# Kernel tuning notes

Measured on AMD Instinct MI355X. Metric: run time of the kernel, lower is better.

## Reference

```python
import jax, jax.numpy as jnp
import numpy as np


def setup_inputs() -> dict:
    key = jax.random.key(0)
    ks = jax.random.split(key, 12)
    B, T, E, H, D, NB, BS = 64, 1, 1280, 20, 64, 7, 64
    w = lambda k: jax.random.normal(k, (E, E), jnp.float32) * 0.02
    return {
        "hidden_states": jax.random.normal(ks[0], (B, T, E), jnp.float32),
        "kcache": jax.random.normal(ks[1], (B, H, NB, BS, D), jnp.float32),
        "vcache": jax.random.normal(ks[2], (B, H, NB, BS, D), jnp.float32),
        "wq": w(ks[3]), "bq": jax.random.normal(ks[4], (E,), jnp.float32) * 0.02,
        "wk": w(ks[5]), "bk": jnp.zeros((E,), jnp.float32),
        "wv": w(ks[6]), "bv": jax.random.normal(ks[7], (E,), jnp.float32) * 0.02,
        "wo": w(ks[8]), "bo": jax.random.normal(ks[9], (E,), jnp.float32) * 0.02,
        "cache_position": jax.random.randint(ks[10], (B,), 0, 447, jnp.int32),
        "block_tables": jax.random.randint(ks[11], (B, NB), 0, NB, jnp.int32),
    }


def reference(hidden_states, kcache, vcache, wq, bq, wk, bk, wv, bv, wo, bo,
              cache_position, block_tables):
    B, T, E = hidden_states.shape          # T == 1 (decode)
    _, H, NB, BS, D = kcache.shape
    L = NB * BS                             # max logical cache length (448)
    scaling = D ** -0.5

    # projections -> (B, H, T, D)
    q = (hidden_states @ wq.T + bq).reshape(B, T, H, D).transpose(0, 2, 1, 3) * scaling
    kn = (hidden_states @ wk.T + bk).reshape(B, T, H, D).transpose(0, 2, 1, 3)
    vn = (hidden_states @ wv.T + bv).reshape(B, T, H, D).transpose(0, 2, 1, 3)

    # paged block-table gather: logical cache (B, H, L, D)
    bt = block_tables[:, None, :, None, None].astype(jnp.int32)
    kc = jnp.take_along_axis(kcache, bt, axis=2).reshape(B, H, L, D)
    vc = jnp.take_along_axis(vcache, bt, axis=2).reshape(B, H, L, D)

    # insert the new token's k/v at position cache_position[b]
    pos = jnp.arange(L, dtype=jnp.int32)
    seq = cache_position.reshape(B, 1, 1, 1)
    at_new = pos.reshape(1, 1, L, 1) == seq          # (B,1,L,1)
    k_full = jnp.where(at_new, kn, kc)               # kn (B,H,1,D) broadcasts
    v_full = jnp.where(at_new, vn, vc)

    # causal decode: attend to positions <= cache_position
    scores = jnp.einsum('bhtd,bhld->bhtl', q, k_full)
    valid = pos.reshape(1, 1, 1, L) <= cache_position.reshape(B, 1, 1, 1)
    scores = jnp.where(valid, scores, jnp.finfo(scores.dtype).min)
    probs = jax.nn.softmax(scores, axis=-1)
    out = jnp.einsum('bhtl,bhld->bhtd', probs, v_full)

    out = out.transpose(0, 2, 1, 3).reshape(B, T, E)
    return out @ wo.T + bo
```

## Files before the change

### kernel.cpp

```cpp
#include <hip/hip_runtime.h>
#include <math.h>

#define E 1280
#define NHEAD 20
#define HD 64
#define NBLK 7
#define NB 64

typedef __bf16 bf16x8 __attribute__((ext_vector_type(8)));
typedef __bf16 bf16x4 __attribute__((ext_vector_type(4)));
typedef float floatx4 __attribute__((ext_vector_type(4)));

__device__ __forceinline__ float wave_max64(float v) {
    #pragma unroll
    for (int o = 32; o > 0; o >>= 1) v = fmaxf(v, __shfl_xor(v, o, 64));
    return v;
}
__device__ __forceinline__ float wave_sum64(float v) {
    #pragma unroll
    for (int o = 32; o > 0; o >>= 1) v += __shfl_xor(v, o, 64);
    return v;
}

template<int NTOT, bool QKV>
__global__ __launch_bounds__(256) void mfma_gemm(
    const float* __restrict__ A,
    const float* __restrict__ W0, const float* __restrict__ W1,
    const float* __restrict__ W2,
    const float* __restrict__ b0, const float* __restrict__ b1,
    const float* __restrict__ b2,
    float* __restrict__ C)
{
    __shared__ __align__(16) __bf16 Asl[64][72];
    __shared__ __align__(16) __bf16 Wsl[16][72];

    const int t = threadIdx.x;
    const int lane = t & 63;
    const int wv = t >> 6;
    const int quad = lane >> 4;
    const int l16 = lane & 15;
    const int jg0 = blockIdx.x * 16;

    int j0; const float* Wp; const float* bp; float scl;
    if (QKV) {
        const int msel = jg0 / E;
        j0 = jg0 - msel * E;
        Wp = (msel == 0) ? W0 : ((msel == 1) ? W1 : W2);
        bp = (msel == 0) ? b0 : ((msel == 1) ? b1 : b2);
        scl = (msel == 0) ? 0.125f : 1.0f;
    } else { j0 = jg0; Wp = W0; bp = b0; scl = 1.0f; }

    const int srow = t >> 4;
    const int sc4 = t & 15;

    floatx4 acc = {0.f, 0.f, 0.f, 0.f};

    for (int k0 = 0; k0 < E; k0 += 64) {
        float4 a4[4];
        #pragma unroll
        for (int r = 0; r < 4; ++r)
            a4[r] = *(const float4*)&A[(size_t)(r * 16 + srow) * E + k0 + sc4 * 4];
        float4 w4 = *(const float4*)&Wp[(size_t)(j0 + srow) * E + k0 + sc4 * 4];

        __syncthreads();
        #pragma unroll
        for (int r = 0; r < 4; ++r) {
            bf16x4 p;
            p[0] = (__bf16)a4[r].x; p[1] = (__bf16)a4[r].y;
            p[2] = (__bf16)a4[r].z; p[3] = (__bf16)a4[r].w;
            *(bf16x4*)&Asl[r * 16 + srow][sc4 * 4] = p;
        }
        {
            bf16x4 p;
            p[0] = (__bf16)w4.x; p[1] = (__bf16)w4.y;
            p[2] = (__bf16)w4.z; p[3] = (__bf16)w4.w;
            *(bf16x4*)&Wsl[srow][sc4 * 4] = p;
        }
        __syncthreads();

        bf16x8 af0 = *(const bf16x8*)&Asl[16 * wv + l16][quad * 8];
        bf16x8 bf0 = *(const bf16x8*)&Wsl[l16][quad * 8];
        acc = __builtin_amdgcn_mfma_f32_16x16x32_bf16(af0, bf0, acc, 0, 0, 0);
        bf16x8 af1 = *(const bf16x8*)&Asl[16 * wv + l16][32 + quad * 8];
        bf16x8 bf1 = *(const bf16x8*)&Wsl[l16][32 + quad * 8];
        acc = __builtin_amdgcn_mfma_f32_16x16x32_bf16(af1, bf1, acc, 0, 0, 0);
    }

    const float bj = bp[j0 + l16];
    #pragma unroll
    for (int r = 0; r < 4; ++r) {
        const int row = 16 * wv + quad * 4 + r;
        C[(size_t)row * NTOT + jg0 + l16] = (acc[r] + bj) * scl;
    }
}

__global__ __launch_bounds__(256) void attn_kernel(
    const float* __restrict__ qkv,
    const float* __restrict__ kcache, const float* __restrict__ vcache,
    const int* __restrict__ cache_position, const int* __restrict__ block_tables,
    float* __restrict__ obuf)
{
    const int bh = blockIdx.x;
    const int b = bh / NHEAD;
    const int h = bh % NHEAD;
    const int lane = threadIdx.x & 63;
    const int wv = threadIdx.x >> 6;
    const int d4 = lane & 15;
    const int sg = lane >> 4;

    __shared__ __align__(16) float q_lds[64];
    __shared__ __align__(16) float o_lds[4][64];
    __shared__ float ml_lds[4][2];

    const int pos = cache_position[b];
    const int last = pos - 1;
    const int col = h * HD + lane;

    const float qd  = qkv[(size_t)b * (3 * E) + col];
    const float knd = qkv[(size_t)b * (3 * E) + E + col];
    const float vnd = qkv[(size_t)b * (3 * E) + 2 * E + col];
    if (wv == 0) q_lds[lane] = qd;
    __syncthreads();

    float m = -INFINITY, lsum = 0.0f;
    float4 vacc = make_float4(0.f, 0.f, 0.f, 0.f);

    for (int nb = wv; nb * 64 <= last; nb += 4) {
        const int phys = block_tables[b * NBLK + nb];
        const size_t boff = ((size_t)((b * NHEAD + h) * NBLK + phys)) << 12;
        const float* __restrict__ Kb = kcache + boff;
        const float* __restrict__ Vb = vcache + boff;

        float sc = 0.0f;
        const float4* Krow = (const float4*)(Kb + lane * HD);
        #pragma unroll
        for (int dd = 0; dd < 16; ++dd) {
            float4 k4 = Krow[dd];
            float4 q4 = ((const float4*)q_lds)[dd];
            sc = fmaf(k4.x, q4.x, sc);
            sc = fmaf(k4.y, q4.y, sc);
            sc = fmaf(k4.z, q4.z, sc);
            sc = fmaf(k4.w, q4.w, sc);
        }
        const int l = nb * 64 + lane;
        if (l > last) sc = -INFINITY;

        const float bm = wave_max64(sc);
        const float mnew = fmaxf(m, bm);
        const float alpha = __expf(m - mnew);
        const float p = __expf(sc - mnew);
        lsum = lsum * alpha + wave_sum64(p);
        vacc.x *= alpha; vacc.y *= alpha; vacc.z *= alpha; vacc.w *= alpha;

        #pragma unroll
        for (int j = 0; j < 16; ++j) {
            const int s = sg + 4 * j;
            const float ps = __shfl(p, s, 64);
            float4 v4 = *(const float4*)&Vb[s * HD + d4 * 4];
            vacc.x = fmaf(ps, v4.x, vacc.x);
            vacc.y = fmaf(ps, v4.y, vacc.y);
            vacc.z = fmaf(ps, v4.z, vacc.z);
            vacc.w = fmaf(ps, v4.w, vacc.w);
        }
        m = mnew;
    }

    #pragma unroll
    for (int o = 16; o <= 32; o <<= 1) {
        vacc.x += __shfl_xor(vacc.x, o, 64);
        vacc.y += __shfl_xor(vacc.y, o, 64);
        vacc.z += __shfl_xor(vacc.z, o, 64);
        vacc.w += __shfl_xor(vacc.w, o, 64);
    }
    if (sg == 0) *(float4*)&o_lds[wv][d4 * 4] = vacc;
    if (lane == 0) { ml_lds[wv][0] = m; ml_lds[wv][1] = lsum; }
    __syncthreads();

    if (wv == 0) {
        const float qk = wave_sum64(qd * knd);
        float Mf = qk;
        #pragma unroll
        for (int w = 0; w < 4; ++w) Mf = fmaxf(Mf, ml_lds[w][0]);
        float osum = 0.0f, Ls = 0.0f;
        #pragma unroll
        for (int w = 0; w < 4; ++w) {
            const float f = __expf(ml_lds[w][0] - Mf);
            osum = fmaf(o_lds[w][lane], f, osum);
            Ls   = fmaf(ml_lds[w][1], f, Ls);
        }
        const float pn = __expf(qk - Mf);
        osum = fmaf(pn, vnd, osum);
        Ls += pn;
        obuf[(size_t)b * E + h * HD + lane] = osum / Ls;
    }
}

extern "C" void kernel_launch(void* const* d_in, const int* in_sizes, int n_in,
                              void* d_out, int out_size, void* d_ws, size_t ws_size,
                              hipStream_t stream) {
    const float* hidden = (const float*)d_in[0];
    const float* kcache = (const float*)d_in[1];
    const float* vcache = (const float*)d_in[2];
    const float* wq = (const float*)d_in[3];
    const float* bq = (const float*)d_in[4];
    const float* wk = (const float*)d_in[5];
    const float* bk = (const float*)d_in[6];
    const float* wvp = (const float*)d_in[7];
    const float* bv = (const float*)d_in[8];
    const float* wo = (const float*)d_in[9];
    const float* bo = (const float*)d_in[10];
    const int* cpos = (const int*)d_in[11];
    const int* btab = (const int*)d_in[12];
    float* out = (float*)d_out;

    float* ws = (float*)d_ws;
    float* qkv = ws;
    float* ob  = ws + 64 * 3 * E;

    mfma_gemm<3 * E, true><<<(3 * E) / 16, 256, 0, stream>>>(
        hidden, wq, wk, wvp, bq, bk, bv, qkv);
    attn_kernel<<<NB * NHEAD, 256, 0, stream>>>(qkv, kcache, vcache, cpos, btab, ob);
    mfma_gemm<E, false><<<E / 16, 256, 0, stream>>>(
        ob, wo, wo, wo, bo, bo, bo, out);
}
```

Measured before the change: 350.8 us.

## Split K across waves in MFMA GEMM with per-wave LDS and final reduction

Each of the four waves in the projection GEMM now handles its own quarter of the K dimension, covering all 64 rows of A with four accumulators. Each wave stages data in a private LDS slice, so the per-iteration block-wide barriers go away. The partial sums are combined through LDS once at the end, and bias and scale are applied there. The trade-off is smaller per-row global load segments (less coalescing), a larger LDS footprint, and an extra reduction step; an empty leftover loop is also left in the code.

```diff
diff --git a/kernel.cpp b/kernel.cpp
--- a/kernel.cpp
+++ b/kernel.cpp
@@ -20,6 +20,12 @@
     #pragma unroll
     for (int o = 32; o > 0; o >>= 1) v += __shfl_xor(v, o, 64);
     return v;
+}
+
+__device__ __forceinline__ bf16x4 cvt4(float4 v) {
+    bf16x4 p;
+    p[0] = (__bf16)v.x; p[1] = (__bf16)v.y; p[2] = (__bf16)v.z; p[3] = (__bf16)v.w;
+    return p;
 }
 
 template<int NTOT, bool QKV>
@@ -31,8 +37,8 @@
     const float* __restrict__ b2,
     float* __restrict__ C)
 {
-    __shared__ __align__(16) __bf16 Asl[64][72];
-    __shared__ __align__(16) __bf16 Wsl[16][72];
+    __shared__ __align__(16) __bf16 Asl[4][64][72];
+    __shared__ __align__(16) __bf16 Wsl[4][16][72];
 
     const int t = threadIdx.x;
     const int lane = t & 63;
@@ -50,47 +56,62 @@
         scl = (msel == 0) ? 0.125f : 1.0f;
     } else { j0 = jg0; Wp = W0; bp = b0; scl = 1.0f; }
 
-    const int srow = t >> 4;
-    const int sc4 = t & 15;
-
-    floatx4 acc = {0.f, 0.f, 0.f, 0.f};
-
-    for (int k0 = 0; k0 < E; k0 += 64) {
-        float4 a4[4];
+    const int sr = lane >> 2;
+    const int sc = lane & 3;
+
+    floatx4 acc[4] = {};
+
+    const int kbeg = wv * (E / 4);
+    for (int c = 0; c < 5; ++c) {
+        const int k0 = kbeg + c * 64;
+        #pragma unroll
+        for (int rg = 0; rg < 4; ++rg) {
+            #pragma unroll
+            for (int cg = 0; cg < 4; ++cg) {
+                float4 v = *(const float4*)&A[(size_t)(rg * 16 + sr) * E + k0 + cg * 16 + sc * 4];
+                *(bf16x4*)&Asl[wv][rg * 16 + sr][cg * 16 + sc * 4] = cvt4(v);
+            }
+        }
+        #pragma unroll
+        for (int cg = 0; cg < 4; ++cg) {
+            float4 v = *(const float4*)&Wp[(size_t)(j0 + sr) * E + k0 + cg * 16 + sc * 4];
+            *(bf16x4*)&Wsl[wv][sr][cg * 16 + sc * 4] = cvt4(v);
+        }
+        bf16x8 bfr0 = *(const bf16x8*)&Wsl[wv][l16][quad * 8];
+        bf16x8 bfr1 = *(const bf16x8*)&Wsl[wv][l16][32 + quad * 8];
+        #pragma unroll
+        for (int rg = 0; rg < 4; ++rg) {
+            bf16x8 af0 = *(const bf16x8*)&Asl[wv][rg * 16 + l16][quad * 8];
+            acc[rg] = __builtin_amdgcn_mfma_f32_16x16x32_bf16(af0, bfr0, acc[rg], 0, 0, 0);
+            bf16x8 af1 = *(const bf16x8*)&Asl[wv][rg * 16 + l16][32 + quad * 8];
+            acc[rg] = __builtin_amdgcn_mfma_f32_16x16x32_bf16(af1, bfr1, acc[rg], 0, 0, 0);
+        }
+    }
+
+    __syncthreads();
+    float (*Cred)[64][16] = (float (*)[64][16])&Asl[0][0][0];
+    #pragma unroll
+    for (int r = 0; r < 4; ++r) {
+        #pragma unroll
+        for (int rg = 0; rg < 4; ++rg)
+            ;
+        ;
+    }
+    #pragma unroll
+    for (int rg = 0; rg < 4; ++rg) {
         #pragma unroll
         for (int r = 0; r < 4; ++r)
-            a4[r] = *(const float4*)&A[(size_t)(r * 16 + srow) * E + k0 + sc4 * 4];
-        float4 w4 = *(const float4*)&Wp[(size_t)(j0 + srow) * E + k0 + sc4 * 4];
-
-        __syncthreads();
-        #pragma unroll
-        for (int r = 0; r < 4; ++r) {
-            bf16x4 p;
-            p[0] = (__bf16)a4[r].x; p[1] = (__bf16)a4[r].y;
-            p[2] = (__bf16)a4[r].z; p[3] = (__bf16)a4[r].w;
-            *(bf16x4*)&Asl[r * 16 + srow][sc4 * 4] = p;
-        }
-        {
-            bf16x4 p;
-            p[0] = (__bf16)w4.x; p[1] = (__bf16)w4.y;
-            p[2] = (__bf16)w4.z; p[3] = (__bf16)w4.w;
-            *(bf16x4*)&Wsl[srow][sc4 * 4] = p;
-        }
-        __syncthreads();
-
-        bf16x8 af0 = *(const bf16x8*)&Asl[16 * wv + l16][quad * 8];
-        bf16x8 bf0 = *(const bf16x8*)&Wsl[l16][quad * 8];
-        acc = __builtin_amdgcn_mfma_f32_16x16x32_bf16(af0, bf0, acc, 0, 0, 0);
-        bf16x8 af1 = *(const bf16x8*)&Asl[16 * wv + l16][32 + quad * 8];
-        bf16x8 bf1 = *(const bf16x8*)&Wsl[l16][32 + quad * 8];
-        acc = __builtin_amdgcn_mfma_f32_16x16x32_bf16(af1, bf1, acc, 0, 0, 0);
-    }
-
-    const float bj = bp[j0 + l16];
-    #pragma unroll
-    for (int r = 0; r < 4; ++r) {
-        const int row = 16 * wv + quad * 4 + r;
-        C[(size_t)row * NTOT + jg0 + l16] = (acc[r] + bj) * scl;
+            Cred[wv][rg * 16 + quad * 4 + r][l16] = acc[rg][r];
+    }
+    __syncthreads();
+
+    #pragma unroll
+    for (int i = 0; i < 4; ++i) {
+        const int e = t + i * 256;
+        const int row = e >> 4, col = e & 15;
+        float s = Cred[0][row][col] + Cred[1][row][col]
+                + Cred[2][row][col] + Cred[3][row][col];
+        C[(size_t)row * NTOT + jg0 + col] = (s + bp[j0 + col]) * scl;
     }
 }
 
```

Result: faster. 338.2 us (-3.6%).
